# Kernel tuning notes

Hardware: AMD Instinct MI355X
Metric: run time of the kernel (lower is better)

The kernel has to match this reference:

```python
import jax, jax.numpy as jnp
import numpy as np

BIG = 1e10  # sentinel for invalid pairwise distances


def get_xyz(depth, fx, fy, cx, cy):
    # depth: [B,1,H,W] -> xyz: [B,3,H,W] via pinhole unprojection
    B, _, H, W = depth.shape
    v = jnp.arange(H, dtype=depth.dtype)[:, None]   # rows
    u = jnp.arange(W, dtype=depth.dtype)[None, :]   # cols
    z = depth[:, 0]                                  # [B,H,W]
    x = (u - cx) / fx * z
    y = (v - cy) / fy * z
    return jnp.stack([x, y, z], axis=1)              # [B,3,H,W]


def _chamfer_item(p, g, vp, vg):
    # p,g: [N,3] point sets; vp,vg: [N] bool validity masks
    # squared pairwise distances via ||p||^2 + ||g||^2 - 2 p.g
    d = (jnp.sum(p * p, -1)[:, None] + jnp.sum(g * g, -1)[None, :]
         - 2.0 * (p @ g.T))                          # [N,N]
    d = jnp.maximum(d, 0.0)
    has_g = jnp.any(vg)
    has_p = jnp.any(vp)
    d1 = jnp.min(jnp.where(vg[None, :], d, BIG), axis=1)  # per pred point
    d2 = jnp.min(jnp.where(vp[:, None], d, BIG), axis=0)  # per gt point
    s1 = jnp.sum(jnp.where(vp & has_g, d1, 0.0))
    s2 = jnp.sum(jnp.where(vg & has_p, d2, 0.0))
    return s1 + s2


def reference(pred, gt_xyz, mask, fx, fy, cx, cy):
    B = pred.shape[0]
    pred_xyz = get_xyz(pred, fx, fy, cx, cy)             # [B,3,H,W]
    p = pred_xyz.reshape(B, 3, -1).transpose(0, 2, 1)    # [B,N,3]
    g = gt_xyz.reshape(B, 3, -1).transpose(0, 2, 1)      # [B,N,3]
    m = mask[:, 0].reshape(B, -1) > 0                    # [B,N]
    # ignore_zeros=True: drop points whose coordinate sum is exactly 0
    vp = m & (jnp.sum(p, -1) != 0)
    vg = m & (jnp.sum(g, -1) != 0)
    per_item = jax.vmap(_chamfer_item)(p, g, vp, vg)     # [B]
    return jnp.sum(per_item) / B


def setup_inputs() -> dict:
    key = jax.random.key(0)
    k1, k2, k3 = jax.random.split(key, 3)
    B, H, W = 2, 128, 128
    pred = jax.random.uniform(k1, (B, 1, H, W), dtype=jnp.float32) * 2.0 + 0.1
    gt_xyz = jax.random.normal(k2, (B, 3, H, W), dtype=jnp.float32)
    mask = jax.random.randint(k3, (B, 1, H, W), 0, 2, dtype=jnp.int32)
    fx = jnp.float32(525.0)
    fy = jnp.float32(525.0)
    cx = jnp.float32(64.0)
    cy = jnp.float32(64.0)
    return {"pred": pred, "gt_xyz": gt_xyz, "mask": mask,
            "fx": fx, "fy": fy, "cx": cx, "cy": cy}
```

## Files before the change

### kernel.cpp

```cpp
#include <hip/hip_runtime.h>

#define B_ITEMS 2
#define W_IMG   128
#define N_PTS   16384
#define CH_GRID 2048
#define BIGF    3.4e38f

__global__ __launch_bounds__(256) void prep_kernel(
        const float* __restrict__ pred,
        const float* __restrict__ gt,
        const int*   __restrict__ mask,
        const float* fxp, const float* fyp,
        const float* cxp, const float* cyp,
        int*    __restrict__ cnt,
        float4* __restrict__ pR, float4* __restrict__ gR,
        float4* __restrict__ pT, float4* __restrict__ gT,
        float*  __restrict__ rmG,
        float*  __restrict__ out) {
    int s    = blockIdx.x >> 6;
    int b    = s & 1;
    int isG  = s >> 1;
    int tid  = threadIdx.x;
    int idx  = (blockIdx.x & 63) * 256 + tid;
    int lane = tid & 63, w = tid >> 6;

    if (blockIdx.x == 0 && tid == 0) out[0] = 0.0f;
    rmG[(blockIdx.x << 8) + tid] = BIGF;

    float x, y, z;
    if (!isG) {
        float fx = *fxp, fy = *fyp, cx = *cxp, cy = *cyp;
        float u = (float)(idx & (W_IMG - 1));
        float v = (float)(idx >> 7);
        z = pred[b * N_PTS + idx];
        x = (u - cx) / fx * z;
        y = (v - cy) / fy * z;
    } else {
        x = gt[(b * 3 + 0) * N_PTS + idx];
        y = gt[(b * 3 + 1) * N_PTS + idx];
        z = gt[(b * 3 + 2) * N_PTS + idx];
    }
    int  mv = mask[b * N_PTS + idx];
    bool ok = (mv > 0) && (((x + y) + z) != 0.0f);

    unsigned long long bal = __ballot(ok);
    int nw  = __popcll(bal);
    int pre = __popcll(bal & ((1ull << lane) - 1ull));

    __shared__ int wbase[4];
    __shared__ int blockbase;
    if (lane == 0) wbase[w] = nw;
    __syncthreads();
    if (tid == 0) {
        int s0 = 0;
#pragma unroll
        for (int i = 0; i < 4; ++i) { int t = wbase[i]; wbase[i] = s0; s0 += t; }
        blockbase = s0 ? atomicAdd(&cnt[s], s0) : 0;
    }
    __syncthreads();

    if (ok) {
        int pos = blockbase + wbase[w] + pre;
        float ps = fmaf(z, z, fmaf(y, y, x * x));
        float4* __restrict__ raw = (isG ? gR : pR) + b * N_PTS;
        float4* __restrict__ tf  = (isG ? gT : pT) + b * N_PTS;
        raw[pos] = make_float4(x, y, z, ps);
        tf[pos]  = make_float4(-2.0f * x, -2.0f * y, -2.0f * z, ps);
    }
}

__global__ __launch_bounds__(256, 4) void chamfer_kernel(
        const int*    __restrict__ cnt,
        const float4* __restrict__ pR, const float4* __restrict__ gR,
        const float4* __restrict__ pT, const float4* __restrict__ gT,
        float* __restrict__ rmG) {
    int np0 = cnt[0], np1 = cnt[1], ng0 = cnt[2], ng1 = cnt[3];
    int naArr[4] = {np0, ng0, np1, ng1};
    int nbArr[4] = {ng0, np0, ng1, np1};
    const float4* Arow[4] = {pR, gR, pR + N_PTS, gR + N_PTS};
    const float4* Bcol[4] = {gT, pT, gT + N_PTS, pT + N_PTS};

    int units[4];
    int Utot = 0;
#pragma unroll
    for (int i = 0; i < 4; ++i) {
        units[i] = (naArr[i] > 0 && nbArr[i] > 0) ? (2 * ((naArr[i] + 63) >> 6)) : 0;
        Utot += units[i];
    }
    int u = blockIdx.x;
    if (u >= Utot) return;
    int s = 0;
    while (u >= units[s]) { u -= units[s]; ++s; }
    int na = naArr[s], nb = nbArr[s];
    const float4* __restrict__ A  = Arow[s];
    const float4* __restrict__ Bp = Bcol[s];
    int h       = u & 1;
    int rowbase = (u >> 1) * 64;
    int half    = (nb + 1) >> 1;
    int cbase   = h * half;
    int ccount  = min(nb - cbase, half);

    int tid = threadIdx.x;
    int tc = tid & 31, tr = tid >> 5;

    float px[8], py[8], pz[8], rm[8];
#pragma unroll
    for (int a = 0; a < 8; ++a) {
        float4 v = A[rowbase + a * 8 + tr];
        px[a] = v.x; py[a] = v.y; pz[a] = v.z;
        rm[a] = BIGF;
    }

    __shared__ float4 sB[2][512];
    int ntiles = (ccount + 511) >> 9;

    if (512 <= ccount) {
#pragma unroll
        for (int k = 0; k < 2; ++k)
            sB[0][k * 256 + tid] = Bp[cbase + k * 256 + tid];
    } else {
#pragma unroll
        for (int k = 0; k < 2; ++k) {
            int j = k * 256 + tid;
            float4 v = Bp[min(cbase + j, N_PTS - 1)];
            bool okc = j < ccount;
            float4 r;
            r.x = okc ? v.x : 0.0f;
            r.y = okc ? v.y : 0.0f;
            r.z = okc ? v.z : 0.0f;
            r.w = okc ? v.w : BIGF;
            sB[0][k * 256 + tid] = r;
        }
    }
    __syncthreads();

    for (int t = 0; t < ntiles; ++t) {
        float4 r0, r1;
        bool have = (t + 1 < ntiles);
        if (have) {
            int j0 = (t + 1) * 512 + tid;
            int j1 = j0 + 256;
            if ((t + 2) * 512 <= ccount) {
                r0 = Bp[cbase + j0];
                r1 = Bp[cbase + j1];
            } else {
                float4 v0 = Bp[min(cbase + j0, N_PTS - 1)];
                float4 v1 = Bp[min(cbase + j1, N_PTS - 1)];
                bool k0 = j0 < ccount, k1 = j1 < ccount;
                r0.x = k0 ? v0.x : 0.0f; r0.y = k0 ? v0.y : 0.0f;
                r0.z = k0 ? v0.z : 0.0f; r0.w = k0 ? v0.w : BIGF;
                r1.x = k1 ? v1.x : 0.0f; r1.y = k1 ? v1.y : 0.0f;
                r1.z = k1 ? v1.z : 0.0f; r1.w = k1 ? v1.w : BIGF;
            }
        }
        const float4* __restrict__ bufc = sB[t & 1] + tc;
#pragma unroll
        for (int cb = 0; cb < 8; ++cb) {
            float4 c0 = bufc[cb * 64];
            float4 c1 = bufc[cb * 64 + 32];
#pragma unroll
            for (int a = 0; a < 8; ++a) {
                float d0 = fmaf(px[a], c0.x,
                              fmaf(py[a], c0.y, fmaf(pz[a], c0.z, c0.w)));
                float d1 = fmaf(px[a], c1.x,
                              fmaf(py[a], c1.y, fmaf(pz[a], c1.z, c1.w)));
                rm[a] = fminf(fminf(rm[a], d0), d1);
            }
        }
        if (have) {
            sB[(t + 1) & 1][tid] = r0;
            sB[(t + 1) & 1][256 + tid] = r1;
        }
        __syncthreads();
    }

#pragma unroll
    for (int a = 0; a < 8; ++a) {
        float v = rm[a];
        v = fminf(v, __shfl_xor(v, 1, 64));
        v = fminf(v, __shfl_xor(v, 2, 64));
        v = fminf(v, __shfl_xor(v, 4, 64));
        v = fminf(v, __shfl_xor(v, 8, 64));
        v = fminf(v, __shfl_xor(v, 16, 64));
        rm[a] = v;
    }
    if (tc == 0) {
        int base = s << 14;
#pragma unroll
        for (int a = 0; a < 8; ++a) {
            int row = rowbase + a * 8 + tr;
            if (row < na) {
                float ps = A[row].w;
                float vr = fmaxf(rm[a] + ps, 0.0f);
                atomicMin((int*)&rmG[base + row], __float_as_int(vr));
            }
        }
    }
}

__global__ __launch_bounds__(256) void finish_kernel(
        const int*   __restrict__ cnt,
        const float* __restrict__ rmG,
        float*       __restrict__ out) {
    int gid = blockIdx.x * 256 + threadIdx.x;
    int s   = gid >> 14;
    int row = gid & (N_PTS - 1);
    int np0 = cnt[0], np1 = cnt[1], ng0 = cnt[2], ng1 = cnt[3];
    int naArr[4] = {np0, ng0, np1, ng1};
    int nbArr[4] = {ng0, np0, ng1, np1};
    float v = (row < naArr[s] && nbArr[s] > 0) ? rmG[gid] : 0.0f;
#pragma unroll
    for (int off = 32; off > 0; off >>= 1)
        v += __shfl_down(v, off, 64);
    __shared__ float wsum[4];
    if ((threadIdx.x & 63) == 0) wsum[threadIdx.x >> 6] = v;
    __syncthreads();
    if (threadIdx.x == 0) {
        float t = (wsum[0] + wsum[1]) + (wsum[2] + wsum[3]);
        atomicAdd(out, t * (1.0f / B_ITEMS));
    }
}

extern "C" void kernel_launch(void* const* d_in, const int* in_sizes, int n_in,
                              void* d_out, int out_size, void* d_ws, size_t ws_size,
                              hipStream_t stream) {
    const float* pred = (const float*)d_in[0];
    const float* gt   = (const float*)d_in[1];
    const int*   mask = (const int*)  d_in[2];
    const float* fx   = (const float*)d_in[3];
    const float* fy   = (const float*)d_in[4];
    const float* cx   = (const float*)d_in[5];
    const float* cy   = (const float*)d_in[6];
    float* out = (float*)d_out;

    char* ws = (char*)d_ws;
    size_t SEG = (size_t)B_ITEMS * N_PTS * 16;
    int*    cnt = (int*)ws;
    float4* pR  = (float4*)(ws + 256);
    float4* gR  = (float4*)(ws + 256 + SEG);
    float4* pT  = (float4*)(ws + 256 + 2 * SEG);
    float4* gT  = (float4*)(ws + 256 + 3 * SEG);
    float*  rmG = (float*) (ws + 256 + 4 * SEG);

    hipMemsetAsync(cnt, 0, 16, stream);

    prep_kernel<<<dim3(256), 256, 0, stream>>>(
        pred, gt, mask, fx, fy, cx, cy, cnt, pR, gR, pT, gT, rmG, out);

    chamfer_kernel<<<dim3(CH_GRID), 256, 0, stream>>>(
        cnt, pR, gR, pT, gT, rmG);

    finish_kernel<<<dim3(256), 256, 0, stream>>>(cnt, rmG, out);
}
```

Baseline: 104.1 us.

## Stage column tiles with direct global-to-LDS loads and a 4-deep ring buffer

Adds a pad kernel that fills each compacted column array up to a multiple of 1024 with sentinel entries, which removes the bounds checks from the chamfer inner loop. Column tiles are then copied straight into LDS with global_load_lds into a 4-slot ring, tracked by explicit vmcnt waits and one barrier per tile in place of the register-staged double buffer. The final per-row atomicMin is also collapsed into one coalesced pass through shared memory. This costs an extra kernel launch and adds reliance on hand-written waitcnt ordering, which is fragile if the compiler reorders memory operations.

After: 100.8 us. -3.2%, faster.

```diff
diff --git a/kernel.cpp b/kernel.cpp
--- a/kernel.cpp
+++ b/kernel.cpp
@@ -3,6 +3,7 @@
 #define B_ITEMS 2
 #define W_IMG   128
 #define N_PTS   16384
+#define QS      2
 #define CH_GRID 2048
 #define BIGF    3.4e38f
 
@@ -69,6 +70,30 @@
     }
 }
 
+__global__ __launch_bounds__(1024) void pad_kernel(
+        const int* __restrict__ cnt,
+        float4* __restrict__ pT, float4* __restrict__ gT) {
+    int s = blockIdx.x;
+    float4* arr = ((s >> 1) ? gT : pT) + (s & 1) * N_PTS;
+    int n = cnt[s];
+    int pos = n + threadIdx.x;
+    if (pos < ((n + 1023) & ~1023))
+        arr[pos] = make_float4(0.0f, 0.0f, 0.0f, BIGF);
+}
+
+#define VMCNT(n) asm volatile("s_waitcnt vmcnt(" #n ")" ::: "memory")
+
+__device__ __forceinline__ void stage_tile(const float4* __restrict__ src,
+                                           float4* lds_base, int w, int lane) {
+    const float4* s0 = src + w * 128 + lane;
+    __builtin_amdgcn_global_load_lds(
+        (const __attribute__((address_space(1))) void*)(s0),
+        (__attribute__((address_space(3))) void*)(lds_base + w * 128), 16, 0, 0);
+    __builtin_amdgcn_global_load_lds(
+        (const __attribute__((address_space(1))) void*)(s0 + 64),
+        (__attribute__((address_space(3))) void*)(lds_base + w * 128 + 64), 16, 0, 0);
+}
+
 __global__ __launch_bounds__(256, 4) void chamfer_kernel(
         const int*    __restrict__ cnt,
         const float4* __restrict__ pR, const float4* __restrict__ gR,
@@ -84,9 +109,10 @@
     int Utot = 0;
 #pragma unroll
     for (int i = 0; i < 4; ++i) {
-        units[i] = (naArr[i] > 0 && nbArr[i] > 0) ? (2 * ((naArr[i] + 63) >> 6)) : 0;
+        units[i] = (naArr[i] > 0 && nbArr[i] > 0) ? (((naArr[i] + 63) >> 6) * QS) : 0;
         Utot += units[i];
     }
+
     int u = blockIdx.x;
     if (u >= Utot) return;
     int s = 0;
@@ -94,14 +120,18 @@
     int na = naArr[s], nb = nbArr[s];
     const float4* __restrict__ A  = Arow[s];
     const float4* __restrict__ Bp = Bcol[s];
-    int h       = u & 1;
+    int q       = u & (QS - 1);
     int rowbase = (u >> 1) * 64;
-    int half    = (nb + 1) >> 1;
-    int cbase   = h * half;
-    int ccount  = min(nb - cbase, half);
-
-    int tid = threadIdx.x;
-    int tc = tid & 31, tr = tid >> 5;
+
+    int nbPad  = (nb + 1023) & ~1023;
+    int Lq     = nbPad >> 1;
+    int cb0    = q * Lq;
+    int ntiles = Lq >> 9;
+
+    int tid  = threadIdx.x;
+    int lane = tid & 63;
+    int w    = tid >> 6;
+    int tc   = tid & 31, tr = tid >> 5;
 
     float px[8], py[8], pz[8], rm[8];
 #pragma unroll
@@ -111,67 +141,39 @@
         rm[a] = BIGF;
     }
 
-    __shared__ float4 sB[2][512];
-    int ntiles = (ccount + 511) >> 9;
-
-    if (512 <= ccount) {
-#pragma unroll
-        for (int k = 0; k < 2; ++k)
-            sB[0][k * 256 + tid] = Bp[cbase + k * 256 + tid];
-    } else {
-#pragma unroll
-        for (int k = 0; k < 2; ++k) {
-            int j = k * 256 + tid;
-            float4 v = Bp[min(cbase + j, N_PTS - 1)];
-            bool okc = j < ccount;
-            float4 r;
-            r.x = okc ? v.x : 0.0f;
-            r.y = okc ? v.y : 0.0f;
-            r.z = okc ? v.z : 0.0f;
-            r.w = okc ? v.w : BIGF;
-            sB[0][k * 256 + tid] = r;
-        }
-    }
-    __syncthreads();
-
+    __shared__ float4 sB[4][512];
+    __shared__ float  smin[64];
+
+    const float4* __restrict__ Bq = Bp + cb0;
+
+    if (0 < ntiles) stage_tile(Bq, sB[0], w, lane);
+    if (1 < ntiles) stage_tile(Bq + 512, sB[1], w, lane);
+    if (2 < ntiles) stage_tile(Bq + 1024, sB[2], w, lane);
+
+#pragma unroll 1
     for (int t = 0; t < ntiles; ++t) {
-        float4 r0, r1;
-        bool have = (t + 1 < ntiles);
-        if (have) {
-            int j0 = (t + 1) * 512 + tid;
-            int j1 = j0 + 256;
-            if ((t + 2) * 512 <= ccount) {
-                r0 = Bp[cbase + j0];
-                r1 = Bp[cbase + j1];
-            } else {
-                float4 v0 = Bp[min(cbase + j0, N_PTS - 1)];
-                float4 v1 = Bp[min(cbase + j1, N_PTS - 1)];
-                bool k0 = j0 < ccount, k1 = j1 < ccount;
-                r0.x = k0 ? v0.x : 0.0f; r0.y = k0 ? v0.y : 0.0f;
-                r0.z = k0 ? v0.z : 0.0f; r0.w = k0 ? v0.w : BIGF;
-                r1.x = k1 ? v1.x : 0.0f; r1.y = k1 ? v1.y : 0.0f;
-                r1.z = k1 ? v1.z : 0.0f; r1.w = k1 ? v1.w : BIGF;
-            }
-        }
-        const float4* __restrict__ bufc = sB[t & 1] + tc;
-#pragma unroll
-        for (int cb = 0; cb < 8; ++cb) {
-            float4 c0 = bufc[cb * 64];
-            float4 c1 = bufc[cb * 64 + 32];
+        int rem = ntiles - 1 - t;
+        if (rem >= 2)      { VMCNT(4); }
+        else if (rem == 1) { VMCNT(2); }
+        else               { VMCNT(0); }
+        __builtin_amdgcn_s_barrier();
+        __builtin_amdgcn_sched_barrier(0);
+        if (t + 3 < ntiles)
+            stage_tile(Bq + (t + 3) * 512, sB[(t + 3) & 3], w, lane);
+        const float4* bufc = &sB[t & 3][tc];
+#pragma unroll
+        for (int cb = 0; cb < 16; cb += 2) {
+            float4 c0 = bufc[cb * 32];
+            float4 c1 = bufc[cb * 32 + 32];
 #pragma unroll
             for (int a = 0; a < 8; ++a) {
                 float d0 = fmaf(px[a], c0.x,
-                              fmaf(py[a], c0.y, fmaf(pz[a], c0.z, c0.w)));
+                             fmaf(py[a], c0.y, fmaf(pz[a], c0.z, c0.w)));
                 float d1 = fmaf(px[a], c1.x,
-                              fmaf(py[a], c1.y, fmaf(pz[a], c1.z, c1.w)));
+                             fmaf(py[a], c1.y, fmaf(pz[a], c1.z, c1.w)));
                 rm[a] = fminf(fminf(rm[a], d0), d1);
             }
         }
-        if (have) {
-            sB[(t + 1) & 1][tid] = r0;
-            sB[(t + 1) & 1][256 + tid] = r1;
-        }
-        __syncthreads();
     }
 
 #pragma unroll
@@ -185,15 +187,17 @@
         rm[a] = v;
     }
     if (tc == 0) {
-        int base = s << 14;
-#pragma unroll
-        for (int a = 0; a < 8; ++a) {
-            int row = rowbase + a * 8 + tr;
-            if (row < na) {
-                float ps = A[row].w;
-                float vr = fmaxf(rm[a] + ps, 0.0f);
-                atomicMin((int*)&rmG[base + row], __float_as_int(vr));
-            }
+#pragma unroll
+        for (int a = 0; a < 8; ++a) smin[a * 8 + tr] = rm[a];
+    }
+    __syncthreads();
+    if (tid < 64) {
+        int row = rowbase + tid;
+        float v  = smin[tid];
+        if (row < na) {
+            float ps = A[row].w;
+            float vr = fmaxf(v + ps, 0.0f);
+            atomicMin((int*)&rmG[(s << 14) + row], __float_as_int(vr));
         }
     }
 }
@@ -247,6 +251,8 @@
     prep_kernel<<<dim3(256), 256, 0, stream>>>(
         pred, gt, mask, fx, fy, cx, cy, cnt, pR, gR, pT, gT, rmG, out);
 
+    pad_kernel<<<dim3(4), 1024, 0, stream>>>(cnt, pT, gT);
+
     chamfer_kernel<<<dim3(CH_GRID), 256, 0, stream>>>(
         cnt, pR, gR, pT, gT, rmG);
 
```
